# Kernel tuning notes

Measured on AMD Instinct MI355X. Metric: run time of the kernel, lower is better.

## Reference

```python
import jax, jax.numpy as jnp
import numpy as np
from jax import lax

H, V, NT, B, T = 1024, 30000, 256, 128, 50
O_ID = 1


def gru_cell(x, h, wih, whh, bih, bhh):
    # PyTorch GRU cell math
    gx = x @ wih.T + bih
    gh = h @ whh.T + bhh
    xr, xz, xn = jnp.split(gx, 3, -1)
    hr, hz, hn = jnp.split(gh, 3, -1)
    r = jax.nn.sigmoid(xr + hr)
    z = jax.nn.sigmoid(xz + hz)
    n = jnp.tanh(xn + r * hn)
    return (1.0 - z) * n + z * h


def masked_scan(xs, mask, wih, whh, bih, bhh):
    # xs [T,B,D], mask [T,B]; emulates pack_padded: padded steps keep hidden, output zeros
    Bn = xs.shape[1]
    Hn = whh.shape[1]
    h0 = jnp.zeros((Bn, Hn), xs.dtype)
    def step(h, inp):
        x, m = inp
        hn = gru_cell(x, h, wih, whh, bih, bhh)
        h_new = jnp.where(m[:, None], hn, h)
        out = jnp.where(m[:, None], hn, 0.0)
        return h_new, out
    h_fin, outs = lax.scan(step, h0, (xs, mask))
    return outs, h_fin


def reverse_padded(xs, lengths):
    # reverse each sequence within its valid length (like pack handles bidirectional)
    Tn = xs.shape[0]
    t = jnp.arange(Tn)[:, None]
    idx = jnp.clip(lengths[None, :] - 1 - t, 0, Tn - 1)  # [T,B]
    return jnp.take_along_axis(xs, idx[:, :, None], axis=0)


def bigru_layer(xs, mask, lengths, wih, whh, bih, bhh):
    out_f, h_f = masked_scan(xs, mask, wih[0], whh[0], bih[0], bhh[0])
    xs_r = reverse_padded(xs, lengths)
    out_bR, h_b = masked_scan(xs_r, mask, wih[1], whh[1], bih[1], bhh[1])
    out_b = reverse_padded(out_bR, lengths) * mask[:, :, None]
    return out_f, out_b, h_f, h_b


def reference(enc_embed, e0_wih, e0_whh, e0_bih, e0_bhh,
              e1_wih, e1_whh, e1_bih, e1_bhh,
              dec_embed, d_wih, d_whh, d_bih, d_bhh,
              concat_w, concat_b, out_w, out_b,
              input_ids, tag_ids, lengths):
    ids = input_ids.T   # [T,B]
    tags = tag_ids.T    # [T,B]
    Tn, Bn = ids.shape
    mask = jnp.arange(Tn)[:, None] < lengths[None, :]  # [T,B]

    # ---- encoder: 2-layer bi-GRU, sum fwd/bwd halves of outputs ----
    emb = enc_embed[ids]  # [T,B,H]
    of0, ob0, h0f, h0b = bigru_layer(emb, mask, lengths, e0_wih, e0_whh, e0_bih, e0_bhh)
    x1 = jnp.concatenate([of0, ob0], -1)  # [T,B,2H]
    of1, ob1, _, _ = bigru_layer(x1, mask, lengths, e1_wih, e1_whh, e1_bih, e1_bhh)
    enc_out = of1 + ob1  # [T,B,H]

    # decoder initial hidden = encoder_hidden[:2] = layer0 fwd, layer0 bwd final states
    dec_in = jnp.concatenate([jnp.full((1, Bn), O_ID, tags.dtype), tags[:-1]], 0)

    def dec_step(carry, tok):
        h0, h1 = carry
        x = dec_embed[tok]                         # [B,H]
        h0 = gru_cell(x, h0, d_wih[0], d_whh[0], d_bih[0], d_bhh[0])
        h1 = gru_cell(h0, h1, d_wih[1], d_whh[1], d_bih[1], d_bhh[1])
        rnn_out = h1
        scores = jnp.einsum('bh,tbh->bt', rnn_out, enc_out)
        attn = jax.nn.softmax(scores, -1)
        ctx = jnp.einsum('bt,tbh->bh', attn, enc_out)
        cc = jnp.tanh(jnp.concatenate([rnn_out, ctx], -1) @ concat_w.T + concat_b)
        logits = cc @ out_w.T + out_b              # [B,NT]
        return (h0, h1), logits

    _, logits = lax.scan(dec_step, (h0f, h0b), dec_in)  # [T,B,NT]

    # masked cross entropy (mean over valid tokens)
    logp = jax.nn.log_softmax(logits, -1)
    nll = -jnp.take_along_axis(logp, tags[..., None].astype(jnp.int32), -1)[..., 0]
    loss = jnp.sum(nll * mask) / jnp.sum(lengths).astype(logits.dtype)

    outputs = jnp.transpose(logits, (1, 0, 2))  # [B,T,NT]
    return outputs, loss


def setup_inputs() -> dict:
    key = jax.random.key(0)
    ks = jax.random.split(key, 24)
    s = 0.05
    inp = {
        'enc_embed': jax.random.normal(ks[0], (V, H)) * s,
        'e0_wih': jax.random.normal(ks[1], (2, 3 * H, H)) * s,
        'e0_whh': jax.random.normal(ks[2], (2, 3 * H, H)) * s,
        'e0_bih': jax.random.normal(ks[3], (2, 3 * H)) * s,
        'e0_bhh': jax.random.normal(ks[4], (2, 3 * H)) * s,
        'e1_wih': jax.random.normal(ks[5], (2, 3 * H, 2 * H)) * s,
        'e1_whh': jax.random.normal(ks[6], (2, 3 * H, H)) * s,
        'e1_bih': jax.random.normal(ks[7], (2, 3 * H)) * s,
        'e1_bhh': jax.random.normal(ks[8], (2, 3 * H)) * s,
        'dec_embed': jax.random.normal(ks[9], (NT, H)) * s,
        'd_wih': jax.random.normal(ks[10], (2, 3 * H, H)) * s,
        'd_whh': jax.random.normal(ks[11], (2, 3 * H, H)) * s,
        'd_bih': jax.random.normal(ks[12], (2, 3 * H)) * s,
        'd_bhh': jax.random.normal(ks[13], (2, 3 * H)) * s,
        'concat_w': jax.random.normal(ks[14], (H, 2 * H)) * s,
        'concat_b': jax.random.normal(ks[15], (H,)) * s,
        'out_w': jax.random.normal(ks[16], (NT, H)) * s,
        'out_b': jax.random.normal(ks[17], (NT,)) * s,
        'input_ids': jax.random.randint(ks[18], (B, T), 0, V, dtype=jnp.int32),
        'tag_ids': jax.random.randint(ks[19], (B, T), 0, NT, dtype=jnp.int32),
    }
    lengths = jax.random.randint(ks[20], (B,), 1, T + 1, dtype=jnp.int32)
    inp['lengths'] = lengths.at[0].set(T)  # max length must equal T
    return inp
```

## Files before the change

kernel.cpp:

```cpp
#include <hip/hip_runtime.h>
#include <math.h>

#define HDIM 1024
#define NTAG 256
#define BSZ 128
#define TLEN 50
#define G3 3072
#define NBLK 256
#define NGRP 8

typedef unsigned long long u64;
typedef unsigned short u16;

constexpr u64 GX_F  = (u64)TLEN*G3*BSZ;
constexpr u64 SEQ_F = (u64)TLEN*HDIM*BSZ;
constexpr u64 HST_F = (u64)HDIM*BSZ;
constexpr u64 F_GX  = 0;
constexpr u64 F_GXB = F_GX + GX_F;
constexpr u64 F_OF0 = F_GXB + GX_F;
constexpr u64 F_OB0 = F_OF0 + SEQ_F;
constexpr u64 F_ENC = F_OB0 + SEQ_F;
constexpr u64 F_ENC2= F_ENC + SEQ_F;
constexpr u64 F_T0  = F_ENC2 + SEQ_F;
constexpr u64 F_T1  = F_T0 + HST_F;
constexpr u64 F_H0F = F_T1 + HST_F;
constexpr u64 F_H0B = F_H0F + HST_F;
constexpr u64 F_X0  = F_H0B + HST_F;
constexpr u64 F_X1  = F_X0 + HST_F;
constexpr u64 F_LG  = F_X1 + HST_F;
constexpr u64 F_QP  = F_LG + (u64)NTAG*BSZ;
constexpr u64 F_NLL = F_QP + (u64)2*TLEN*BSZ;
constexpr u64 F_H1T = F_NLL + (u64)TLEN*BSZ;
constexpr u64 F_CWB = F_H1T + 65536;
constexpr u64 F_OWB = F_CWB + 1048576;
constexpr u64 F_ETB = F_OWB + 131072;
constexpr u64 SHU   = 65536;
constexpr u64 F_SH0A= F_ETB + 3276800;
constexpr u64 F_SH0B= F_SH0A + SHU;
constexpr u64 F_SH1A= F_SH0B + SHU;
constexpr u64 F_SH1B= F_SH1A + SHU;
constexpr u64 F_SCTX= F_SH1B + SHU;
constexpr u64 F_SCC = F_SCTX + SHU;
constexpr u64 F_SHI0= F_SCC + SHU;
constexpr u64 F_SHI1= F_SHI0 + SHU;
constexpr u64 POOL_F= F_SHI1 + SHU;

__device__ __align__(256) float g_pool[POOL_F];
__device__ unsigned g_grp[NGRP*32];
__device__ unsigned g_root;
__device__ unsigned g_gen;
__device__ unsigned g2_grp[2*NGRP*32];
__device__ unsigned g2_root[2*32];
__device__ unsigned g2_gen[2*32];

__device__ __forceinline__ float sigmf(float x){ return 1.f/(1.f+__expf(-x)); }
__device__ __forceinline__ u16 f2b(float x){
  unsigned u = __float_as_uint(x);
  u += 0x7fffu + ((u>>16)&1u);
  return (u16)(u>>16);
}
__device__ __forceinline__ float b2f(u16 s){ return __uint_as_float(((unsigned)s)<<16); }
__device__ __forceinline__ float b2f_lo(unsigned p){ return __uint_as_float(p<<16); }
__device__ __forceinline__ float b2f_hi(unsigned p){ return __uint_as_float(p & 0xffff0000u); }

__device__ __forceinline__ void grid_sync(){
  __syncthreads();
  if (threadIdx.x == 0){
    const int g = blockIdx.x & (NGRP-1);
    unsigned gen = __hip_atomic_load(&g_gen, __ATOMIC_RELAXED, __HIP_MEMORY_SCOPE_AGENT);
    unsigned old = __hip_atomic_fetch_add(&g_grp[g*32], 1u, __ATOMIC_RELEASE, __HIP_MEMORY_SCOPE_AGENT);
    if (old == (NBLK/NGRP)-1){
      unsigned ro = __hip_atomic_fetch_add(&g_root, 1u, __ATOMIC_RELEASE, __HIP_MEMORY_SCOPE_AGENT);
      if (ro == NGRP-1){
        __hip_atomic_store(&g_root, 0u, __ATOMIC_RELAXED, __HIP_MEMORY_SCOPE_AGENT);
        #pragma unroll
        for (int i=0;i<NGRP;++i)
          __hip_atomic_store(&g_grp[i*32], 0u, __ATOMIC_RELAXED, __HIP_MEMORY_SCOPE_AGENT);
        __hip_atomic_fetch_add(&g_gen, 1u, __ATOMIC_RELEASE, __HIP_MEMORY_SCOPE_AGENT);
      } else {
        while (__hip_atomic_load(&g_gen, __ATOMIC_RELAXED, __HIP_MEMORY_SCOPE_AGENT) == gen)
          __builtin_amdgcn_s_sleep(4);
      }
    } else {
      while (__hip_atomic_load(&g_gen, __ATOMIC_RELAXED, __HIP_MEMORY_SCOPE_AGENT) == gen)
        __builtin_amdgcn_s_sleep(4);
    }
    (void)__hip_atomic_load(&g_gen, __ATOMIC_ACQUIRE, __HIP_MEMORY_SCOPE_AGENT);
  }
  __syncthreads();
}

__device__ __forceinline__ void grid_sync_h(int half){
  __syncthreads();
  if (threadIdx.x == 0){
    const int g = (blockIdx.x & 255) & (NGRP-1);
    unsigned* grp  = &g2_grp[(half*NGRP + g)*32];
    unsigned* root = &g2_root[half*32];
    unsigned* genp = &g2_gen[half*32];
    unsigned gen = __hip_atomic_load(genp, __ATOMIC_RELAXED, __HIP_MEMORY_SCOPE_AGENT);
    unsigned old = __hip_atomic_fetch_add(grp, 1u, __ATOMIC_RELEASE, __HIP_MEMORY_SCOPE_AGENT);
    if (old == (NBLK/NGRP)-1){
      unsigned ro = __hip_atomic_fetch_add(root, 1u, __ATOMIC_RELEASE, __HIP_MEMORY_SCOPE_AGENT);
      if (ro == NGRP-1){
        __hip_atomic_store(root, 0u, __ATOMIC_RELAXED, __HIP_MEMORY_SCOPE_AGENT);
        #pragma unroll
        for (int i=0;i<NGRP;++i)
          __hip_atomic_store(&g2_grp[(half*NGRP + i)*32], 0u, __ATOMIC_RELAXED, __HIP_MEMORY_SCOPE_AGENT);
        __hip_atomic_fetch_add(genp, 1u, __ATOMIC_RELEASE, __HIP_MEMORY_SCOPE_AGENT);
      } else {
        while (__hip_atomic_load(genp, __ATOMIC_RELAXED, __HIP_MEMORY_SCOPE_AGENT) == gen)
          __builtin_amdgcn_s_sleep(4);
      }
    } else {
      while (__hip_atomic_load(genp, __ATOMIC_RELAXED, __HIP_MEMORY_SCOPE_AGENT) == gen)
        __builtin_amdgcn_s_sleep(4);
    }
    (void)__hip_atomic_load(genp, __ATOMIC_ACQUIRE, __HIP_MEMORY_SCOPE_AGENT);
  }
  __syncthreads();
}

__device__ __forceinline__ void ggemm12u(const u16* __restrict__ wl,
                                         const u16* __restrict__ aT,
                                         float (&acc)[12][2], int tid)
{
  const int w = tid>>6, l2 = (tid&63)*2;
  #pragma unroll
  for (int r=0;r<12;++r){ acc[r][0]=0.f; acc[r][1]=0.f; }
  const int k0 = w*128;
  const u16* ap = aT + (u64)k0*BSZ + l2;
  const u16* wp = wl + k0*12;
  for (int kb=0; kb<128; kb+=16){
    unsigned a[16];
    #pragma unroll
    for (int u=0;u<16;++u) a[u] = *(const unsigned*)(ap + (u64)(kb+u)*BSZ);
    #pragma unroll
    for (int u=0;u<16;++u){
      const u16* wr = wp + (kb+u)*12;
      const float ax = b2f_lo(a[u]), ay = b2f_hi(a[u]);
      #pragma unroll
      for (int r=0;r<12;++r){
        const float wv = b2f(wr[r]);
        acc[r][0] += wv*ax; acc[r][1] += wv*ay;
      }
    }
  }
}

__device__ __forceinline__ void reduce12(const float (&acc)[12][2], float* red, int tid){
  const int w = tid>>6, l2 = (tid&63)*2;
  __syncthreads();
  #pragma unroll
  for (int r=0;r<12;++r){
    red[(u64)(w*12+r)*128 + l2]   = acc[r][0];
    red[(u64)(w*12+r)*128 + l2+1] = acc[r][1];
  }
  __syncthreads();
}

#define AM_ENC 0
#define AM_DEC 1
#define AM_CAT 2

template<int AMODE>
__global__ __launch_bounds__(256)
void gemm_gx(const float* __restrict__ embed,
             u64 a1_f, u64 a2_f,
             const int* __restrict__ ids,
             const float* __restrict__ W,
             const float* __restrict__ bias,
             u64 c_f, int K)
{
  constexpr int TM=128, TN=64, TK=32;
  __shared__ float As[TK][TM+4];
  __shared__ float Ws[TK][TN+4];
  __shared__ int rowid[TM];
  const int t = blockIdx.x;
  const int n0 = blockIdx.y*TN;
  const int tid = threadIdx.x;

  if (AMODE != AM_CAT){
    for (int r=tid; r<TM; r+=256)
      rowid[r] = (AMODE==AM_ENC) ? ids[r*TLEN+t] : ((t==0)?1:ids[r*TLEN+t-1]);
    __syncthreads();
  }

  const int tm = tid>>4, tn = tid&15;
  float acc[8][4];
  #pragma unroll
  for (int i=0;i<8;i++){ acc[i][0]=0.f;acc[i][1]=0.f;acc[i][2]=0.f;acc[i][3]=0.f; }

  for (int k0=0;k0<K;k0+=TK){
    if (AMODE==AM_CAT){
      const int kk = tid>>3, q = tid&7;
      const int kg = k0 + kk;
      const float* src = g_pool + ((kg<HDIM)? (a1_f + ((u64)t*HDIM + kg)*BSZ)
                                            : (a2_f + ((u64)t*HDIM + (kg-HDIM))*BSZ)) + q*16;
      float* d = &As[kk][q*16];
      float4 v0=*(const float4*)(src+0), v1=*(const float4*)(src+4);
      float4 v2=*(const float4*)(src+8), v3=*(const float4*)(src+12);
      *(float4*)(d+0)=v0; *(float4*)(d+4)=v1; *(float4*)(d+8)=v2; *(float4*)(d+12)=v3;
    } else {
      #pragma unroll
      for (int l=tid; l<TM*TK; l+=256){
        int r=l>>5, k=l&31;
        As[k][r] = embed[(u64)rowid[r]*HDIM + k0 + k];
      }
    }
    #pragma unroll
    for (int l=tid; l<TN*TK; l+=256){
      int n=l>>5, k=l&31;
      Ws[k][n] = W[(u64)(n0+n)*K + k0 + k];
    }
    __syncthreads();
    #pragma unroll 8
    for (int kk=0;kk<TK;kk++){
      float4 a0 = *(const float4*)&As[kk][tm*8];
      float4 a1 = *(const float4*)&As[kk][tm*8+4];
      float4 w  = *(const float4*)&Ws[kk][tn*4];
      float av[8]={a0.x,a0.y,a0.z,a0.w,a1.x,a1.y,a1.z,a1.w};
      float wv[4]={w.x,w.y,w.z,w.w};
      #pragma unroll
      for (int i=0;i<8;i++){
        #pragma unroll
        for (int jj=0;jj<4;jj++) acc[i][jj] += av[i]*wv[jj];
      }
    }
    __syncthreads();
  }

  float bv[4];
  #pragma unroll
  for (int jj=0;jj<4;jj++) bv[jj] = bias[n0+tn*4+jj];
  float* C = g_pool + c_f;
  for (int half=0; half<2; ++half){
    if ((tn>>3)==half){
      #pragma unroll
      for (int i=0;i<8;i++)
        #pragma unroll
        for (int jj=0;jj<4;jj++)
          As[(tn&7)*4+jj][tm*8+i] = acc[i][jj]+bv[jj];
    }
    __syncthreads();
    {
      const int nn = tid>>3, q = tid&7;
      float* dst = C + ((u64)t*G3 + n0 + half*32 + nn)*BSZ + q*16;
      const float* srow = &As[nn][q*16];
      float4 v0=*(const float4*)(srow+0), v1=*(const float4*)(srow+4);
      float4 v2=*(const float4*)(srow+8), v3=*(const float4*)(srow+12);
      *(float4*)(dst+0)=v0; *(float4*)(dst+4)=v1; *(float4*)(dst+8)=v2; *(float4*)(dst+12)=v3;
    }
    __syncthreads();
  }
}

__device__ __forceinline__ void ggemm12(const u16* __restrict__ wl,
                                        const float* __restrict__ aT,
                                        float (&acc)[12][2], int tid)
{
  const int w = tid>>6, l2 = (tid&63)*2;
  #pragma unroll
  for (int r=0;r<12;++r){ acc[r][0]=0.f; acc[r][1]=0.f; }
  const int k0 = w*128;
  const float* ap = aT + (u64)k0*BSZ + l2;
  const u16* wp = wl + k0*12;
  for (int kb=0; kb<128; kb+=16){
    float2 a[16];
    #pragma unroll
    for (int u=0;u<16;++u) a[u] = *(const float2*)(ap + (u64)(kb+u)*BSZ);
    #pragma unroll
    for (int u=0;u<16;++u){
      const u16* wr = wp + (kb+u)*12;
      #pragma unroll
      for (int r=0;r<12;++r){
        const float wv = b2f(wr[r]);
        acc[r][0] += wv*a[u].x; acc[r][1] += wv*a[u].y;
      }
    }
  }
}

__global__ __launch_bounds__(512)
void scan_pair(u64 gxA, u64 gxB, u64 p0A, u64 p1A, u64 p0B, u64 p1B,
               const float* __restrict__ whhA, const float* __restrict__ whhB,
               const float* __restrict__ bhhA, const float* __restrict__ bhhB,
               const int* __restrict__ lengths, u64 outA, u64 outB)
{
  __shared__ u16 wl[HDIM*12];
  __shared__ float red[8*12*128];
  const int gbid = blockIdx.x, tid = threadIdx.x;
  const int half = gbid >> 8;
  const int bid  = gbid & 255;
  const u64 gx_f = half? gxB : gxA;
  const u64 p0_f = half? p0B : p0A;
  const u64 p1_f = half? p1B : p1A;
  const float* whh = half? whhB : whhA;
  const float* bhh = half? bhhB : bhhA;
  const u64 out_f = half? outB : outA;
  const bool bwd = (half != 0);

  const int j0 = bid*4;
  #pragma unroll
  for (int r=0;r<12;++r){
    const int row = (r>>2)*HDIM + j0 + (r&3);
    for (int k=tid;k<HDIM;k+=512) wl[k*12+r] = f2b(whh[(u64)row*HDIM + k]);
  }
  __syncthreads();

  const int jl = tid>>7, bb = tid&127;
  const int jg = j0 + jl;
  for (int s=0; s<TLEN; ++s){
    const int t = bwd ? (TLEN-1-s) : s;
    const u64 rd = (s&1)? p0_f : p1_f;
    const u64 wr = (s&1)? p1_f : p0_f;
    if (s>0){
      float acc[12][2];
      ggemm12(wl, g_pool + rd, acc, tid);
      reduce12(acc, red, tid);
    }
    const float* gxb = g_pool + gx_f + (u64)t*G3*BSZ;
    {
      const int len = lengths[bb];
      const bool m = (t < len);
      float gh0=0.f, gh1=0.f, gh2=0.f;
      if (s>0){
        #pragma unroll
        for (int w2=0;w2<8;++w2){
          gh0 += red[(u64)(w2*12 + jl)*128 + bb];
          gh1 += red[(u64)(w2*12 + 4 + jl)*128 + bb];
          gh2 += red[(u64)(w2*12 + 8 + jl)*128 + bb];
        }
      }
      const float xr = gxb[(u64)jg*BSZ + bb];
      const float xz = gxb[(u64)(HDIM+jg)*BSZ + bb];
      const float xn = gxb[(u64)(2*HDIM+jg)*BSZ + bb];
      const float hp = (s>0)? g_pool[rd + (u64)jg*BSZ + bb] : 0.f;
      const float r = sigmf(xr + gh0 + bhh[jg]);
      const float z = sigmf(xz + gh1 + bhh[HDIM+jg]);
      const float n = tanhf(xn + r*(gh2 + bhh[2*HDIM+jg]));
      const float hv = (1.f-z)*n + z*hp;
      g_pool[wr + (u64)jg*BSZ + bb] = m ? hv : hp;
      g_pool[out_f + ((u64)t*HDIM + jg)*BSZ + bb] = m ? hv : 0.f;
    }
    grid_sync_h(half);
  }
}

__global__ __launch_bounds__(256)
void conv_w(const float* __restrict__ cw, const float* __restrict__ ow){
  u16* cwb = (u16*)(g_pool + F_CWB);
  u16* owb = (u16*)(g_pool + F_OWB);
  u16* hi0 = (u16*)(g_pool + F_SHI0);
  u16* hi1 = (u16*)(g_pool + F_SHI1);
  const u64 n1 = (u64)HDIM*2*HDIM;
  const u64 n2 = (u64)NTAG*HDIM;
  const u64 n3 = (u64)HDIM*BSZ;
  for (u64 i = (u64)blockIdx.x*256+threadIdx.x; i<n1; i += (u64)gridDim.x*256) cwb[i]=f2b(cw[i]);
  for (u64 i = (u64)blockIdx.x*256+threadIdx.x; i<n2; i += (u64)gridDim.x*256) owb[i]=f2b(ow[i]);
  for (u64 i = (u64)blockIdx.x*256+threadIdx.x; i<n3; i += (u64)gridDim.x*256){
    hi0[i]=f2b(g_pool[F_H0F + i]);
    hi1[i]=f2b(g_pool[F_H0B + i]);
  }
}
__global__ __launch_bounds__(256)
void enc_t(){
  const int t = blockIdx.x, kc = blockIdx.y;
  u16* etb = (u16*)(g_pool + F_ETB);
  for (int it=threadIdx.x; it<128*128; it+=256){
    const int kl = it>>7, b = it&127;
    const int k = kc*128 + kl;
    const u64 idx = ((u64)t*HDIM+k)*BSZ + b;
    etb[(u64)b*(TLEN*HDIM) + (u64)t*HDIM + k] = f2b(g_pool[F_ENC + idx] + g_pool[F_ENC2 + idx]);
  }
}

__global__ __launch_bounds__(512)
void decoder_kernel(const float* __restrict__ whh0, const float* __restrict__ bhh0,
                    const float* __restrict__ wih1, const float* __restrict__ bih1,
                    const float* __restrict__ whh1, const float* __restrict__ bhh1,
                    const float* __restrict__ cb, const float* __restrict__ ob,
                    const int* __restrict__ tag_ids, const int* __restrict__ lengths,
                    float* __restrict__ dout)
{
  __shared__ u16 wl0[HDIM*12];
  __shared__ u16 wl1[HDIM*12];
  __shared__ u16 wl2[HDIM*12];
  __shared__ float red[8*12*128];
  __shared__ float aL[64];
  const int bid = blockIdx.x, tid = threadIdx.x;
  const int j0 = bid*4;
  const int ab = bid>>1, kh2 = bid&1;
  const int w = tid>>6, l2 = (tid&63)*2, l = tid&63;
  const int jl = tid>>7, bb = tid&127;
  const int jg = j0 + jl;

  #pragma unroll
  for (int r=0;r<12;++r){
    const int gr = (r>>2)*HDIM + j0 + (r&3);
    for (int k=tid;k<HDIM;k+=512){
      wl0[k*12+r] = f2b(whh0[(u64)gr*HDIM + k]);
      wl1[k*12+r] = f2b(wih1[(u64)gr*HDIM + k]);
      wl2[k*12+r] = f2b(whh1[(u64)gr*HDIM + k]);
    }
  }
  __syncthreads();

  u16* h1t = (u16*)(g_pool + F_H1T);
  const u16* etb = (const u16*)(g_pool + F_ETB);
  const u16* cwb = (const u16*)(g_pool + F_CWB);
  const u16* owb = (const u16*)(g_pool + F_OWB);
  u16* sctx = (u16*)(g_pool + F_SCTX);
  u16* scc  = (u16*)(g_pool + F_SCC);

  for (int t=0; t<TLEN; ++t){
    const u16* h0c = (const u16*)(g_pool + ((t==0)? F_SHI0 : ((t&1)? F_SH0A : F_SH0B)));
    u16*       h0n = (u16*)(g_pool + ((t&1)? F_SH0B : F_SH0A));
    const u16* h1c = (const u16*)(g_pool + ((t==0)? F_SHI1 : ((t&1)? F_SH1A : F_SH1B)));
    u16*       h1n = (u16*)(g_pool + ((t&1)? F_SH1B : F_SH1A));

    {
      float acc[12][2];
      ggemm12u(wl0, h0c, acc, tid);
      reduce12(acc, red, tid);
      const float* gxb = g_pool + F_GX + (u64)t*G3*BSZ;
      float gh0=0.f, gh1=0.f, gh2=0.f;
      #pragma unroll
      for (int w2=0;w2<8;++w2){
        gh0 += red[(u64)(w2*12 + jl)*128 + bb];
        gh1 += red[(u64)(w2*12 + 4 + jl)*128 + bb];
        gh2 += red[(u64)(w2*12 + 8 + jl)*128 + bb];
      }
      const float xr = gxb[(u64)jg*BSZ+bb], xz = gxb[(u64)(HDIM+jg)*BSZ+bb], xn = gxb[(u64)(2*HDIM+jg)*BSZ+bb];
      const float hp = b2f(h0c[(u64)jg*BSZ + bb]);
      const float r = sigmf(xr + gh0 + bhh0[jg]);
      const float z = sigmf(xz + gh1 + bhh0[HDIM+jg]);
      const float n = tanhf(xn + r*(gh2 + bhh0[2*HDIM+jg]));
      h0n[(u64)jg*BSZ + bb] = f2b((1.f-z)*n + z*hp);
    }
    grid_sync();

    {
      float acc[12][2];
      float aX[3], aH[3];
      ggemm12u(wl1, h0n, acc, tid);
      reduce12(acc, red, tid);
      #pragma unroll
      for (int g=0;g<3;++g){
        float s=0.f;
        #pragma unroll
        for (int w2=0;w2<8;++w2) s += red[(u64)(w2*12 + g*4 + jl)*128 + bb];
        aX[g] = s;
      }
      ggemm12u(wl2, h1c, acc, tid);
      reduce12(acc, red, tid);
      #pragma unroll
      for (int g=0;g<3;++g){
        float s=0.f;
        #pragma unroll
        for (int w2=0;w2<8;++w2) s += red[(u64)(w2*12 + g*4 + jl)*128 + bb];
        aH[g] = s;
      }
      const float hp = b2f(h1c[(u64)jg*BSZ + bb]);
      const float r = sigmf(aX[0] + bih1[jg] + aH[0] + bhh1[jg]);
      const float z = sigmf(aX[1] + bih1[HDIM+jg] + aH[1] + bhh1[HDIM+jg]);
      const float n = tanhf(aX[2] + bih1[2*HDIM+jg] + r*(aH[2] + bhh1[2*HDIM+jg]));
      const float hv = (1.f-z)*n + z*hp;
      const u16 hb = f2b(hv);
      h1n[(u64)jg*BSZ + bb] = hb;
      h1t[(u64)bb*HDIM + jg] = hb;
    }
    grid_sync();

    {
      const u16* h1r = h1t + (u64)ab*HDIM + kh2*512 + l*8;
      float hv[8];
      #pragma unroll
      for (int u=0;u<8;++u) hv[u] = b2f(h1r[u]);
      for (int tp=w; tp<TLEN; tp+=8){
        const u16* er = etb + (u64)ab*(TLEN*HDIM) + (u64)tp*HDIM + kh2*512 + l*8;
        float s=0.f;
        #pragma unroll
        for (int u=0;u<8;++u) s += hv[u]*b2f(er[u]);
        #pragma unroll
        for (int o=32;o;o>>=1) s += __shfl_xor(s, o);
        if (l==0) g_pool[F_QP + (u64)kh2*TLEN*BSZ + (u64)tp*BSZ + ab] = s;
      }
    }
    grid_sync();

    {
      if (tid < 64){
        float v = -1e30f;
        if (tid < TLEN)
          v = g_pool[F_QP + (u64)tid*BSZ + ab] + g_pool[F_QP + (u64)(TLEN+tid)*BSZ + ab];
        float mx = v;
        #pragma unroll
        for (int o=32;o;o>>=1) mx = fmaxf(mx, __shfl_xor(mx,o));
        float e = (tid<TLEN)? __expf(v-mx) : 0.f;
        float sm = e;
        #pragma unroll
        for (int o=32;o;o>>=1) sm += __shfl_xor(sm,o);
        if (tid < TLEN) aL[tid] = e/sm;
      }
      __syncthreads();
      {
        const int kk = tid;
        const u16* eb = etb + (u64)ab*(TLEN*HDIM) + kh2*512 + kk;
        float acc = 0.f;
        #pragma unroll 10
        for (int tp=0;tp<TLEN;++tp) acc += aL[tp]*b2f(eb[(u64)tp*HDIM]);
        sctx[(u64)(kh2*512+kk)*BSZ + ab] = f2b(acc);
      }
    }
    grid_sync();

    {
      const int k0 = w*256;
      const u16* asrc = (k0<1024)? ((const u16*)(g_pool + ((t&1)? F_SH1B : F_SH1A)) + (u64)k0*BSZ)
                                 : (sctx + (u64)(k0-1024)*BSZ);
      const u16* wp0 = cwb + (u64)(j0+0)*2048 + k0;
      const u16* wp1 = cwb + (u64)(j0+1)*2048 + k0;
      const u16* wp2 = cwb + (u64)(j0+2)*2048 + k0;
      const u16* wp3 = cwb + (u64)(j0+3)*2048 + k0;
      float a0[4]={0,0,0,0}, a1v[4]={0,0,0,0};
      for (int kb=0; kb<256; kb+=16){
        unsigned a[16];
        #pragma unroll
        for (int u=0;u<16;++u) a[u] = *(const unsigned*)(asrc + (u64)(kb+u)*BSZ + l2);
        #pragma unroll
        for (int u=0;u<16;++u){
          const float ax = b2f_lo(a[u]), ay = b2f_hi(a[u]);
          const float w0v=b2f(wp0[kb+u]), w1v=b2f(wp1[kb+u]), w2v=b2f(wp2[kb+u]), w3v=b2f(wp3[kb+u]);
          a0[0]+=w0v*ax; a1v[0]+=w0v*ay;
          a0[1]+=w1v*ax; a1v[1]+=w1v*ay;
          a0[2]+=w2v*ax; a1v[2]+=w2v*ay;
          a0[3]+=w3v*ax; a1v[3]+=w3v*ay;
        }
      }
      __syncthreads();
      #pragma unroll
      for (int r=0;r<4;++r){
        red[(u64)(w*4+r)*128 + l2]   = a0[r];
        red[(u64)(w*4+r)*128 + l2+1] = a1v[r];
      }
      __syncthreads();
      {
        const int n2 = j0 + jl;
        float s = cb[n2];
        #pragma unroll
        for (int w2=0;w2<8;++w2) s += red[(u64)(w2*4+jl)*128 + bb];
        scc[(u64)n2*BSZ + bb] = f2b(tanhf(s));
      }
    }
    grid_sync();

    {
      const u16* owv = owb + (u64)bid*HDIM + w*128;
      const u16* ccp = scc + (u64)w*128*BSZ;
      float a0=0.f, a1v=0.f;
      for (int kb=0; kb<128; kb+=16){
        unsigned a[16];
        #pragma unroll
        for (int u=0;u<16;++u) a[u] = *(const unsigned*)(ccp + (u64)(kb+u)*BSZ + l2);
        #pragma unroll
        for (int u=0;u<16;++u){
          const float wv = b2f(owv[kb+u]);
          a0 += wv*b2f_lo(a[u]); a1v += wv*b2f_hi(a[u]);
        }
      }
      __syncthreads();
      red[(u64)w*128 + l2]   = a0;
      red[(u64)w*128 + l2+1] = a1v;
      __syncthreads();
      if (tid < 128){
        float lg = ob[bid];
        #pragma unroll
        for (int w2=0;w2<8;++w2) lg += red[(u64)w2*128 + tid];
        g_pool[F_LG + (u64)bid*BSZ + tid] = lg;
      }
    }
    grid_sync();

    {
      float* lgs = red;
      float* rp  = red + 256;
      const bool act = (bid < BSZ) && (tid < 256);
      float lg = 0.f;
      if (act){
        lg = g_pool[F_LG + (u64)tid*BSZ + bid];
        lgs[tid] = lg; rp[tid] = lg;
      }
      __syncthreads();
      for (int o=128;o;o>>=1){ if (bid<BSZ && tid<o) rp[tid]=fmaxf(rp[tid],rp[tid+o]); __syncthreads(); }
      const float mx = (bid<BSZ)? rp[0] : 0.f;
      __syncthreads();
      if (act) rp[tid] = __expf(lg-mx);
      __syncthreads();
      for (int o=128;o;o>>=1){ if (bid<BSZ && tid<o) rp[tid]+=rp[tid+o]; __syncthreads(); }
      if (act){
        const float lse = mx + __logf(rp[0]);
        dout[((u64)bid*TLEN + t)*NTAG + tid] = lg;
        if (tid==0){
          const int tag = tag_ids[bid*TLEN + t];
          g_pool[F_NLL + (u64)t*BSZ + bid] = lse - lgs[tag];
        }
      }
    }
  }
  grid_sync();
  if (bid == 0){
    float ssum = 0.f;
    for (int i=tid; i<TLEN*BSZ; i+=512){
      const int tt = i>>7, b = i&127;
      if (tt < lengths[b]) ssum += g_pool[F_NLL + i];
    }
    red[tid] = ssum; __syncthreads();
    for (int o=256;o;o>>=1){ if (tid<o) red[tid]+=red[tid+o]; __syncthreads(); }
    if (tid==0){
      int den=0;
      for (int b=0;b<BSZ;b++) den += lengths[b];
      dout[(u64)BSZ*TLEN*NTAG] = red[0]/(float)den;
    }
  }
}

extern "C" void kernel_launch(void* const* d_in, const int* in_sizes, int n_in,
                              void* d_out, int out_size, void* d_ws, size_t ws_size,
                              hipStream_t stream)
{
  const float* enc_embed = (const float*)d_in[0];
  const float* e0_wih = (const float*)d_in[1];
  const float* e0_whh = (const float*)d_in[2];
  const float* e0_bih = (const float*)d_in[3];
  const float* e0_bhh = (const float*)d_in[4];
  const float* e1_wih = (const float*)d_in[5];
  const float* e1_whh = (const float*)d_in[6];
  const float* e1_bih = (const float*)d_in[7];
  const float* e1_bhh = (const float*)d_in[8];
  const float* dec_embed = (const float*)d_in[9];
  const float* d_wih = (const float*)d_in[10];
  const float* d_whh = (const float*)d_in[11];
  const float* d_bih = (const float*)d_in[12];
  const float* d_bhh = (const float*)d_in[13];
  const float* concat_w = (const float*)d_in[14];
  const float* concat_b = (const float*)d_in[15];
  const float* out_w = (const float*)d_in[16];
  const float* out_b = (const float*)d_in[17];
  const int* input_ids = (const int*)d_in[18];
  const int* tag_ids  = (const int*)d_in[19];
  const int* lengths  = (const int*)d_in[20];
  float* dout = (float*)d_out;

  const dim3 gxg(TLEN, G3/64);

  gemm_gx<AM_ENC><<<gxg,256,0,stream>>>(enc_embed,0,0,input_ids,e0_wih,e0_bih,F_GX,HDIM);
  gemm_gx<AM_ENC><<<gxg,256,0,stream>>>(enc_embed,0,0,input_ids,
                                        e0_wih+(u64)G3*HDIM, e0_bih+G3, F_GXB, HDIM);
  scan_pair<<<2*NBLK,512,0,stream>>>(F_GX, F_GXB, F_T0, F_H0F, F_T1, F_H0B,
                                     e0_whh, e0_whh+(u64)G3*HDIM, e0_bhh, e0_bhh+G3,
                                     lengths, F_OF0, F_OB0);
  gemm_gx<AM_CAT><<<gxg,256,0,stream>>>(nullptr, F_OF0, F_OB0, nullptr,
                                        e1_wih, e1_bih, F_GX, 2*HDIM);
  gemm_gx<AM_CAT><<<gxg,256,0,stream>>>(nullptr, F_OF0, F_OB0, nullptr,
                                        e1_wih+(u64)G3*2*HDIM, e1_bih+G3, F_GXB, 2*HDIM);
  scan_pair<<<2*NBLK,512,0,stream>>>(F_GX, F_GXB, F_T0, F_X0, F_T1, F_X1,
                                     e1_whh, e1_whh+(u64)G3*HDIM, e1_bhh, e1_bhh+G3,
                                     lengths, F_ENC, F_ENC2);
  gemm_gx<AM_DEC><<<gxg,256,0,stream>>>(dec_embed,0,0,tag_ids, d_wih, d_bih, F_GX, HDIM);
  conv_w<<<256,256,0,stream>>>(concat_w, out_w);
  enc_t<<<dim3(TLEN,8),256,0,stream>>>();
  decoder_kernel<<<NBLK,512,0,stream>>>(d_whh, d_bhh,
                                        d_wih+(u64)G3*HDIM, d_bih+G3,
                                        d_whh+(u64)G3*HDIM, d_bhh+G3,
                                        concat_b, out_b,
                                        tag_ids, lengths, dout);
}
```

Baseline: 17.09 ms.

## Store gate pre-activations as bf16 and cache encoder slice in decoder LDS

The gx GEMM now writes its output as packed bf16 instead of fp32, which halves the gx buffers and the per-step reads in the encoder and decoder recurrences. In the decoder, the reduction buffer is halved by reducing in two passes of four waves each. The freed LDS holds the block's encoder-output slice, so the attention score and context loops read from shared memory instead of global memory on every step. This trades some precision on the pre-activations and adds extra barriers in the reduction.

```diff
diff --git a/kernel.cpp b/kernel.cpp
--- a/kernel.cpp
+++ b/kernel.cpp
@@ -12,12 +12,12 @@
 typedef unsigned long long u64;
 typedef unsigned short u16;
 
-constexpr u64 GX_F  = (u64)TLEN*G3*BSZ;
+constexpr u64 GXU   = (u64)TLEN*G3*BSZ/2;
 constexpr u64 SEQ_F = (u64)TLEN*HDIM*BSZ;
 constexpr u64 HST_F = (u64)HDIM*BSZ;
 constexpr u64 F_GX  = 0;
-constexpr u64 F_GXB = F_GX + GX_F;
-constexpr u64 F_OF0 = F_GXB + GX_F;
+constexpr u64 F_GXB = F_GX + GXU;
+constexpr u64 F_OF0 = F_GXB + GXU;
 constexpr u64 F_OB0 = F_OF0 + SEQ_F;
 constexpr u64 F_ENC = F_OB0 + SEQ_F;
 constexpr u64 F_ENC2= F_ENC + SEQ_F;
@@ -158,6 +158,45 @@
   __syncthreads();
 }
 
+__device__ __forceinline__ void reduce12_2p(const float (&acc)[12][2], float* red, int tid,
+                                            int jl, int bb, float (&gh)[3])
+{
+  const int w = tid>>6, l2 = (tid&63)*2;
+  gh[0]=0.f; gh[1]=0.f; gh[2]=0.f;
+  __syncthreads();
+  if (w < 4){
+    #pragma unroll
+    for (int r=0;r<12;++r){
+      red[(u64)(w*12+r)*128 + l2]   = acc[r][0];
+      red[(u64)(w*12+r)*128 + l2+1] = acc[r][1];
+    }
+  }
+  __syncthreads();
+  #pragma unroll
+  for (int g=0;g<3;++g){
+    float s=0.f;
+    #pragma unroll
+    for (int w2=0;w2<4;++w2) s += red[(u64)(w2*12 + g*4 + jl)*128 + bb];
+    gh[g] += s;
+  }
+  __syncthreads();
+  if (w >= 4){
+    #pragma unroll
+    for (int r=0;r<12;++r){
+      red[(u64)((w-4)*12+r)*128 + l2]   = acc[r][0];
+      red[(u64)((w-4)*12+r)*128 + l2+1] = acc[r][1];
+    }
+  }
+  __syncthreads();
+  #pragma unroll
+  for (int g=0;g<3;++g){
+    float s=0.f;
+    #pragma unroll
+    for (int w2=0;w2<4;++w2) s += red[(u64)(w2*12 + g*4 + jl)*128 + bb];
+    gh[g] += s;
+  }
+}
+
 #define AM_ENC 0
 #define AM_DEC 1
 #define AM_CAT 2
@@ -232,7 +271,7 @@
   float bv[4];
   #pragma unroll
   for (int jj=0;jj<4;jj++) bv[jj] = bias[n0+tn*4+jj];
-  float* C = g_pool + c_f;
+  u16* C16 = (u16*)(g_pool + c_f);
   for (int half=0; half<2; ++half){
     if ((tn>>3)==half){
       #pragma unroll
@@ -244,11 +283,14 @@
     __syncthreads();
     {
       const int nn = tid>>3, q = tid&7;
-      float* dst = C + ((u64)t*G3 + n0 + half*32 + nn)*BSZ + q*16;
+      u16* dst = C16 + ((u64)t*G3 + n0 + half*32 + nn)*BSZ + q*16;
       const float* srow = &As[nn][q*16];
-      float4 v0=*(const float4*)(srow+0), v1=*(const float4*)(srow+4);
-      float4 v2=*(const float4*)(srow+8), v3=*(const float4*)(srow+12);
-      *(float4*)(dst+0)=v0; *(float4*)(dst+4)=v1; *(float4*)(dst+8)=v2; *(float4*)(dst+12)=v3;
+      unsigned pk[8];
+      #pragma unroll
+      for (int i=0;i<8;++i)
+        pk[i] = (unsigned)f2b(srow[2*i]) | ((unsigned)f2b(srow[2*i+1])<<16);
+      *(uint4*)(dst)   = make_uint4(pk[0],pk[1],pk[2],pk[3]);
+      *(uint4*)(dst+8) = make_uint4(pk[4],pk[5],pk[6],pk[7]);
     }
     __syncthreads();
   }
@@ -318,7 +360,7 @@
       ggemm12(wl, g_pool + rd, acc, tid);
       reduce12(acc, red, tid);
     }
-    const float* gxb = g_pool + gx_f + (u64)t*G3*BSZ;
+    const u16* gxb = (const u16*)(g_pool + gx_f) + (u64)t*G3*BSZ;
     {
       const int len = lengths[bb];
       const bool m = (t < len);
@@ -331,9 +373,9 @@
           gh2 += red[(u64)(w2*12 + 8 + jl)*128 + bb];
         }
       }
-      const float xr = gxb[(u64)jg*BSZ + bb];
-      const float xz = gxb[(u64)(HDIM+jg)*BSZ + bb];
-      const float xn = gxb[(u64)(2*HDIM+jg)*BSZ + bb];
+      const float xr = b2f(gxb[(u64)jg*BSZ + bb]);
+      const float xz = b2f(gxb[(u64)(HDIM+jg)*BSZ + bb]);
+      const float xn = b2f(gxb[(u64)(2*HDIM+jg)*BSZ + bb]);
       const float hp = (s>0)? g_pool[rd + (u64)jg*BSZ + bb] : 0.f;
       const float r = sigmf(xr + gh0 + bhh[jg]);
       const float z = sigmf(xz + gh1 + bhh[HDIM+jg]);
@@ -385,7 +427,8 @@
   __shared__ u16 wl0[HDIM*12];
   __shared__ u16 wl1[HDIM*12];
   __shared__ u16 wl2[HDIM*12];
-  __shared__ float red[8*12*128];
+  __shared__ float red[4*12*128];
+  __shared__ u16 encL[TLEN*512];
   __shared__ float aL[64];
   const int bid = blockIdx.x, tid = threadIdx.x;
   const int j0 = bid*4;
@@ -403,14 +446,21 @@
       wl2[k*12+r] = f2b(whh1[(u64)gr*HDIM + k]);
     }
   }
+  {
+    const u16* src = (const u16*)(g_pool + F_ETB) + (u64)ab*(TLEN*HDIM) + kh2*512;
+    for (int idx=tid; idx<TLEN*256; idx+=512){
+      const int tp = idx >> 8, kk2 = (idx & 255)*2;
+      *(unsigned*)&encL[tp*512 + kk2] = *(const unsigned*)(src + (u64)tp*HDIM + kk2);
+    }
+  }
   __syncthreads();
 
   u16* h1t = (u16*)(g_pool + F_H1T);
-  const u16* etb = (const u16*)(g_pool + F_ETB);
   const u16* cwb = (const u16*)(g_pool + F_CWB);
   const u16* owb = (const u16*)(g_pool + F_OWB);
   u16* sctx = (u16*)(g_pool + F_SCTX);
   u16* scc  = (u16*)(g_pool + F_SCC);
+  const u16* gxall = (const u16*)(g_pool + F_GX);
 
   for (int t=0; t<TLEN; ++t){
     const u16* h0c = (const u16*)(g_pool + ((t==0)? F_SHI0 : ((t&1)? F_SH0A : F_SH0B)));
@@ -421,20 +471,16 @@
     {
       float acc[12][2];
       ggemm12u(wl0, h0c, acc, tid);
-      reduce12(acc, red, tid);
-      const float* gxb = g_pool + F_GX + (u64)t*G3*BSZ;
-      float gh0=0.f, gh1=0.f, gh2=0.f;
-      #pragma unroll
-      for (int w2=0;w2<8;++w2){
-        gh0 += red[(u64)(w2*12 + jl)*128 + bb];
-        gh1 += red[(u64)(w2*12 + 4 + jl)*128 + bb];
-        gh2 += red[(u64)(w2*12 + 8 + jl)*128 + bb];
-      }
-      const float xr = gxb[(u64)jg*BSZ+bb], xz = gxb[(u64)(HDIM+jg)*BSZ+bb], xn = gxb[(u64)(2*HDIM+jg)*BSZ+bb];
+      float gh[3];
+      reduce12_2p(acc, red, tid, jl, bb, gh);
+      const u16* gxb = gxall + (u64)t*G3*BSZ;
+      const float xr = b2f(gxb[(u64)jg*BSZ+bb]);
+      const float xz = b2f(gxb[(u64)(HDIM+jg)*BSZ+bb]);
+      const float xn = b2f(gxb[(u64)(2*HDIM+jg)*BSZ+bb]);
       const float hp = b2f(h0c[(u64)jg*BSZ + bb]);
-      const float r = sigmf(xr + gh0 + bhh0[jg]);
-      const float z = sigmf(xz + gh1 + bhh0[HDIM+jg]);
-      const float n = tanhf(xn + r*(gh2 + bhh0[2*HDIM+jg]));
+      const float r = sigmf(xr + gh[0] + bhh0[jg]);
+      const float z = sigmf(xz + gh[1] + bhh0[HDIM+jg]);
+      const float n = tanhf(xn + r*(gh[2] + bhh0[2*HDIM+jg]));
       h0n[(u64)jg*BSZ + bb] = f2b((1.f-z)*n + z*hp);
     }
     grid_sync();
@@ -443,23 +489,9 @@
       float acc[12][2];
       float aX[3], aH[3];
       ggemm12u(wl1, h0n, acc, tid);
-      reduce12(acc, red, tid);
-      #pragma unroll
-      for (int g=0;g<3;++g){
-        float s=0.f;
-        #pragma unroll
-        for (int w2=0;w2<8;++w2) s += red[(u64)(w2*12 + g*4 + jl)*128 + bb];
-        aX[g] = s;
-      }
+      reduce12_2p(acc, red, tid, jl, bb, aX);
       ggemm12u(wl2, h1c, acc, tid);
-      reduce12(acc, red, tid);
-      #pragma unroll
-      for (int g=0;g<3;++g){
-        float s=0.f;
-        #pragma unroll
-        for (int w2=0;w2<8;++w2) s += red[(u64)(w2*12 + g*4 + jl)*128 + bb];
-        aH[g] = s;
-      }
+      reduce12_2p(acc, red, tid, jl, bb, aH);
       const float hp = b2f(h1c[(u64)jg*BSZ + bb]);
       const float r = sigmf(aX[0] + bih1[jg] + aH[0] + bhh1[jg]);
       const float z = sigmf(aX[1] + bih1[HDIM+jg] + aH[1] + bhh1[HDIM+jg]);
@@ -477,7 +509,7 @@
       #pragma unroll
       for (int u=0;u<8;++u) hv[u] = b2f(h1r[u]);
       for (int tp=w; tp<TLEN; tp+=8){
-        const u16* er = etb + (u64)ab*(TLEN*HDIM) + (u64)tp*HDIM + kh2*512 + l*8;
+        const u16* er = &encL[tp*512 + l*8];
         float s=0.f;
         #pragma unroll
         for (int u=0;u<8;++u) s += hv[u]*b2f(er[u]);
@@ -505,10 +537,9 @@
       __syncthreads();
       {
         const int kk = tid;
-        const u16* eb = etb + (u64)ab*(TLEN*HDIM) + kh2*512 + kk;
         float acc = 0.f;
         #pragma unroll 10
-        for (int tp=0;tp<TLEN;++tp) acc += aL[tp]*b2f(eb[(u64)tp*HDIM]);
+        for (int tp=0;tp<TLEN;++tp) acc += aL[tp]*b2f(encL[tp*512 + kk]);
         sctx[(u64)(kh2*512+kk)*BSZ + ab] = f2b(acc);
       }
     }
```

Measured after the change: 17.43 ms. Within noise of the previous version (+2.0%).
